# Kernel optimization log

Measured on AMD Instinct MI355X. Metric: run time of the kernel, lower is better.

The kernel has to match this reference:

```python
import jax, jax.numpy as jnp
import numpy as np

B, T = 1, 2048
N_HEAD = 16
N_KV_HEAD = 16
N_EMBD = 1024
HEAD_DIM = N_EMBD // N_HEAD  # 64
HD8 = HEAD_DIM // 8          # 8 octonion blocks per head
EPS_RMS = 1e-6


def qconj(q):
    return q * jnp.array([1.0, -1.0, -1.0, -1.0], dtype=q.dtype)


def qmul(q1, q2):
    # Hamilton product, (...,4) x (...,4) -> (...,4)
    w1, x1, y1, z1 = (q1[..., 0], q1[..., 1], q1[..., 2], q1[..., 3])
    w2, x2, y2, z2 = (q2[..., 0], q2[..., 1], q2[..., 2], q2[..., 3])
    return jnp.stack([
        w1 * w2 - x1 * x2 - y1 * y2 - z1 * z2,
        w1 * x2 + x1 * w2 + y1 * z2 - z1 * y2,
        w1 * y2 - x1 * z2 + y1 * w2 + z1 * x2,
        w1 * z2 + x1 * y2 - y1 * x2 + z1 * w2,
    ], axis=-1)


def omul(o1, o2):
    # Cayley-Dickson octonion product, (...,8)
    a, b = o1[..., :4], o1[..., 4:]
    c, d = o2[..., :4], o2[..., 4:]
    first = qmul(a, c) - qmul(qconj(d), b)
    second = qmul(d, a) + qmul(b, qconj(c))
    return jnp.concatenate([first, second], axis=-1)


def oconj(o):
    return jnp.concatenate([qconj(o[..., :4]), -o[..., 4:]], axis=-1)


# Octonion multiplication structure constants: omul(x, y)[k] = x[a] y[p] C[a,p,k]
_EYE8 = jnp.eye(8, dtype=jnp.float32)
C_OCT = jax.vmap(lambda ei: jax.vmap(lambda ej: omul(ei, ej))(_EYE8))(_EYE8)  # (8,8,8)
# Trilinear tensor for omul(omul(q, kc), v):  T3[a,p,q,k] = sum_e C[a,p,e] C[e,q,k]
T3 = jnp.einsum('ape,eqk->apqk', C_OCT, C_OCT)  # (8,8,8,8)


def apply_rotary_emb(x, cos, sin):
    # x: (B, T, H, hd); cos/sin: (1, T, 1, hd//2)
    d = x.shape[-1] // 2
    x1, x2 = x[..., :d], x[..., d:]
    y1 = x1 * cos + x2 * sin
    y2 = x2 * cos - x1 * sin
    return jnp.concatenate([y1, y2], axis=-1)


def rms_norm(x):
    return x * jax.lax.rsqrt(jnp.mean(x * x, axis=-1, keepdims=True) + EPS_RMS)


def setup_inputs() -> dict:
    key = jax.random.key(0)
    ks = jax.random.split(key, 7)
    x = jax.random.normal(ks[0], (B, T, N_EMBD), dtype=jnp.float32)
    cos = jax.random.uniform(ks[1], (1, T, 1, HEAD_DIM // 2), dtype=jnp.float32)
    sin = jax.random.uniform(ks[2], (1, T, 1, HEAD_DIM // 2), dtype=jnp.float32)
    s = 0.02
    Wq = jax.random.normal(ks[3], (N_HEAD * HEAD_DIM, N_EMBD), dtype=jnp.float32) * s
    Wk = jax.random.normal(ks[4], (N_KV_HEAD * HEAD_DIM, N_EMBD), dtype=jnp.float32) * s
    Wv = jax.random.normal(ks[5], (N_KV_HEAD * HEAD_DIM, N_EMBD), dtype=jnp.float32) * s
    Wo = jax.random.normal(ks[6], (N_EMBD, N_EMBD), dtype=jnp.float32) * s
    return {"x": x, "cos": cos, "sin": sin, "Wq": Wq, "Wk": Wk, "Wv": Wv, "Wo": Wo}


def reference(x, cos, sin, Wq, Wk, Wv, Wo):
    Bx, Tx, Cx = x.shape
    q = (x @ Wq.T).reshape(Bx, Tx, N_HEAD, HEAD_DIM)
    k = (x @ Wk.T).reshape(Bx, Tx, N_KV_HEAD, HEAD_DIM)
    v = (x @ Wv.T).reshape(Bx, Tx, N_KV_HEAD, HEAD_DIM)
    q = rms_norm(apply_rotary_emb(q, cos, sin))
    k = rms_norm(apply_rotary_emb(k, cos, sin))
    q = q.transpose(0, 2, 1, 3)  # (B,H,T,hd)
    k = k.transpose(0, 2, 1, 3)
    v = v.transpose(0, 2, 1, 3)

    q_o = q.reshape(Bx, N_HEAD, Tx, HD8, 8)
    k_o = k.reshape(Bx, N_KV_HEAD, Tx, HD8, 8)
    v_o = v.reshape(Bx, N_KV_HEAD, Tx, HD8, 8)
    # F.normalize(p=2, dim=-1): divide by max(||.||, 1e-12)
    k_o = k_o / jnp.maximum(jnp.linalg.norm(k_o, axis=-1, keepdims=True), 1e-12)

    # Scores use the (pre-octonion-normalized) rotary+rms k
    scores = jnp.einsum('bhid,bhjd->bhij', q, k) * (HEAD_DIM ** -0.5)
    mask = jnp.tril(jnp.ones((Tx, Tx), dtype=bool))
    scores = jnp.where(mask, scores, -jnp.inf)
    probs = jax.nn.softmax(scores, axis=-1)  # (B,H,Tq,Tk)

    # y_i = sum_j p_ij * omul(omul(q_i, oconj(k_j)), v_j)
    # omul is bilinear, so pull the j-sum inside:
    # y_i[k] = q_i[a] * T3[a,p,c,k] * (sum_j p_ij kc_j[p] v_j[c])
    kc = oconj(k_o)                                              # (B,H,Tk,M,8)
    KV = jnp.einsum('bhjmp,bhjmq->bhjmpq', kc, v_o)              # (B,H,Tk,M,8,8)
    Z = jnp.einsum('bhij,bhjmpq->bhimpq', probs, KV)             # (B,H,Tq,M,8,8)
    y_o = jnp.einsum('bhima,apqk,bhimpq->bhimk', q_o, T3, Z)     # (B,H,Tq,M,8)

    y = y_o.reshape(Bx, N_HEAD, Tx, HEAD_DIM).transpose(0, 2, 1, 3).reshape(Bx, Tx, Cx)
    return y @ Wo.T
```

## Files before the change

kernel.cpp:

```cpp
#include <hip/hip_runtime.h>

typedef unsigned short u16;
typedef unsigned int u32;

#define T_SEQ 2048
#define NHEAD 16
#define HDIM 64
#define CDIM 1024
#define W_HSTR (512*2048)
#define Z_HSTR (2048*512)

#define SGBITS 0xB2D8741EACC66A00ULL

#define EXP2C 0.18033688011112042f

typedef _Float16 f16x8 __attribute__((ext_vector_type(8)));
typedef float f32x4 __attribute__((ext_vector_type(4)));

__device__ __forceinline__ float h2f(u16 u) { _Float16 h; __builtin_memcpy(&h, &u, 2); return (float)h; }
__device__ __forceinline__ u16 f2h(float f) { _Float16 h = (_Float16)f; u16 u; __builtin_memcpy(&u, &h, 2); return u; }
__device__ __forceinline__ u32 pk(float a, float b) { return (u32)f2h(a) | ((u32)f2h(b) << 16); }

__device__ __forceinline__ void gload16(const u16* g, u16* l) {
    __builtin_amdgcn_global_load_lds((const __attribute__((address_space(1))) u32*)g,
                                     (__attribute__((address_space(3))) u32*)l, 16, 0, 0);
}

template<bool F16OUT>
__device__ __forceinline__ void hgemm_tile(const u16* __restrict__ At, int lda,
                                           const u16* __restrict__ Bt, int ldb, int K,
                                           float* __restrict__ Cf, u16* __restrict__ Ch,
                                           int ldc, float scale, u16* As, u16* Bs) {
    int t = threadIdx.x;
    int wave = t >> 6, l = t & 63;
    int wm = wave & 1, wn = wave >> 1;
    int quad = l >> 4, lr = l & 15;
    f32x4 acc[4][4];
#pragma unroll
    for (int i = 0; i < 4; ++i)
#pragma unroll
        for (int j = 0; j < 4; ++j) acc[i][j] = (f32x4){0.f, 0.f, 0.f, 0.f};
    int acol = quad * 8;
    for (int k0 = 0; k0 < K; k0 += 64) {
#pragma unroll
        for (int j = 0; j < 4; ++j) {
            int d = wave * 4 + j;
            int kb = d >> 3, seg = d & 7;
            size_t roff = (size_t)(seg * 16 + lr);
            int coff = k0 + kb * 32 + acol;
            gload16(At + roff * lda + coff, As + d * 512);
            gload16(Bt + roff * ldb + coff, Bs + d * 512);
        }
        __syncthreads();
#pragma unroll
        for (int kb = 0; kb < 2; ++kb) {
            f16x8 af[4], bf[4];
#pragma unroll
            for (int mi = 0; mi < 4; ++mi) af[mi] = *(const f16x8*)&As[(kb * 8 + wm * 4 + mi) * 512 + l * 8];
#pragma unroll
            for (int ni = 0; ni < 4; ++ni) bf[ni] = *(const f16x8*)&Bs[(kb * 8 + wn * 4 + ni) * 512 + l * 8];
#pragma unroll
            for (int mi = 0; mi < 4; ++mi)
#pragma unroll
                for (int ni = 0; ni < 4; ++ni)
                    acc[mi][ni] = __builtin_amdgcn_mfma_f32_16x16x32_f16(af[mi], bf[ni], acc[mi][ni], 0, 0, 0);
        }
        __syncthreads();
    }
#pragma unroll
    for (int mi = 0; mi < 4; ++mi)
#pragma unroll
        for (int ni = 0; ni < 4; ++ni)
#pragma unroll
            for (int rr = 0; rr < 4; ++rr) {
                int gr = wm * 64 + mi * 16 + quad * 4 + rr;
                int gc = wn * 64 + ni * 16 + lr;
                float v = acc[mi][ni][rr] * scale;
                if (F16OUT) Ch[(size_t)gr * ldc + gc] = f2h(v);
                else Cf[(size_t)gr * ldc + gc] = v;
            }
}

__global__ __launch_bounds__(256) void hgemm_f32(const u16* __restrict__ A, int lda,
                                                 const u16* __restrict__ B, int ldb,
                                                 float* __restrict__ C, int ldc, int K) {
    __shared__ u16 As[8192], Bs[8192];
    int bm = blockIdx.y * 128, bn = blockIdx.x * 128;
    hgemm_tile<false>(A + (size_t)bm * lda, lda, B + (size_t)bn * ldb, ldb, K,
                      C + (size_t)bm * ldc + bn, nullptr, ldc, 1.f, As, Bs);
}

__global__ __launch_bounds__(256) void hgemm_f16(const u16* __restrict__ A, int lda,
                                                 const u16* __restrict__ B, int ldb,
                                                 u16* __restrict__ C, int ldc, int K) {
    __shared__ u16 As[8192], Bs[8192];
    int bm = blockIdx.y * 128, bn = blockIdx.x * 128;
    hgemm_tile<true>(A + (size_t)bm * lda, lda, B + (size_t)bn * ldb, ldb, K,
                     nullptr, C + (size_t)bm * ldc + bn, ldc, 1.f, As, Bs);
}

__global__ __launch_bounds__(256, 2) void flash_pw(const u16* __restrict__ q16,
                                                   const u16* __restrict__ k16,
                                                   const u16* __restrict__ W,
                                                   u16* __restrict__ Z,
                                                   float* __restrict__ lbuf) {
    __shared__ u16 Pl[2][128 * 136];
    int idx = blockIdx.x;
    int rb = 15 - (idx >> 6);
    int i6 = idx & 63;
    int h = ((i6 & 7) << 1) | ((i6 >> 3) & 1);
    int nq = i6 >> 4;
    int t = threadIdx.x;
    int wave = t >> 6, l = t & 63;
    int wm = wave & 1, wn = wave >> 1;
    int quad = l >> 4, lr = l & 15;

    const u16* qbase = q16 + (size_t)(rb * 128 + wm * 64 + lr) * CDIM + h * HDIM + quad * 8;
    f16x8 qa[4][2];
#pragma unroll
    for (int mi = 0; mi < 4; ++mi)
#pragma unroll
        for (int kb = 0; kb < 2; ++kb)
            qa[mi][kb] = *(const f16x8*)(qbase + (size_t)(mi * 16) * CDIM + kb * 32);

    f32x4 accz[4][4];
    f32x4 accl[4];
#pragma unroll
    for (int mi = 0; mi < 4; ++mi) {
        accl[mi] = (f32x4){0.f, 0.f, 0.f, 0.f};
#pragma unroll
        for (int ni = 0; ni < 4; ++ni) accz[mi][ni] = (f32x4){0.f, 0.f, 0.f, 0.f};
    }
    f16x8 ones;
#pragma unroll
    for (int j = 0; j < 8; ++j) ones[j] = (_Float16)1.0f;

    const u16* kbase = k16 + (size_t)(wn * 64 + lr) * CDIM + h * HDIM + quad * 8;
    const u16* Wbase = W + (size_t)h * W_HSTR + (size_t)(nq * 128 + wn * 64 + lr) * T_SEQ + quad * 8;

    auto qk = [&](int cb, f32x4 (&s)[4][4]) {
        f16x8 kf[4][2];
#pragma unroll
        for (int ni = 0; ni < 4; ++ni)
#pragma unroll
            for (int kb = 0; kb < 2; ++kb)
                kf[ni][kb] = *(const f16x8*)(kbase + (size_t)(cb * 128 + ni * 16) * CDIM + kb * 32);
#pragma unroll
        for (int mi = 0; mi < 4; ++mi)
#pragma unroll
            for (int ni = 0; ni < 4; ++ni) s[mi][ni] = (f32x4){0.f, 0.f, 0.f, 0.f};
#pragma unroll
        for (int kb = 0; kb < 2; ++kb)
#pragma unroll
            for (int mi = 0; mi < 4; ++mi)
#pragma unroll
                for (int ni = 0; ni < 4; ++ni)
                    s[mi][ni] = __builtin_amdgcn_mfma_f32_16x16x32_f16(qa[mi][kb], kf[ni][kb], s[mi][ni], 0, 0, 0);
    };
    auto expst = [&](int cb, f32x4 (&s)[4][4], u16* Pd) {
#pragma unroll
        for (int mi = 0; mi < 4; ++mi) {
            int row = wm * 64 + mi * 16 + quad * 4;
#pragma unroll
            for (int ni = 0; ni < 4; ++ni) {
                int col = wn * 64 + ni * 16 + lr;
#pragma unroll
                for (int rr = 0; rr < 4; ++rr) {
                    bool valid = (cb < rb) | (col <= row + rr);
                    float p = valid ? __builtin_amdgcn_exp2f(s[mi][ni][rr] * EXP2C - 12.f) : 0.f;
                    Pd[(row + rr) * 136 + col] = f2h(p);
                }
            }
        }
    };
    auto pw = [&](int cb, const u16* Ps) {
#pragma unroll
        for (int kb = 0; kb < 4; ++kb) {
            f16x8 pf[4], wf[4];
#pragma unroll
            for (int ni = 0; ni < 4; ++ni)
                wf[ni] = *(const f16x8*)(Wbase + (size_t)(ni * 16) * T_SEQ + cb * 128 + kb * 32);
#pragma unroll
            for (int mi = 0; mi < 4; ++mi)
                pf[mi] = *(const f16x8*)&Ps[(wm * 64 + mi * 16 + lr) * 136 + kb * 32 + quad * 8];
#pragma unroll
            for (int mi = 0; mi < 4; ++mi) {
#pragma unroll
                for (int ni = 0; ni < 4; ++ni)
                    accz[mi][ni] = __builtin_amdgcn_mfma_f32_16x16x32_f16(pf[mi], wf[ni], accz[mi][ni], 0, 0, 0);
                if (nq == 0)
                    accl[mi] = __builtin_amdgcn_mfma_f32_16x16x32_f16(pf[mi], ones, accl[mi], 0, 0, 0);
            }
        }
    };

    {
        f32x4 s[4][4];
        qk(0, s);
        expst(0, s, Pl[0]);
    }
    int cur = 0;
    for (int cb = 1; cb <= rb; ++cb) {
        __syncthreads();
        f32x4 s[4][4];
        qk(cb, s);
        pw(cb - 1, Pl[cur]);
        expst(cb, s, Pl[cur ^ 1]);
        cur ^= 1;
    }
    __syncthreads();
    pw(rb, Pl[cur]);

    u16* Zb = Z + (size_t)h * Z_HSTR;
#pragma unroll
    for (int mi = 0; mi < 4; ++mi)
#pragma unroll
        for (int rr = 0; rr < 4; ++rr) {
            int row = rb * 128 + wm * 64 + mi * 16 + quad * 4 + rr;
#pragma unroll
            for (int ni = 0; ni < 4; ++ni) {
                int col = nq * 128 + wn * 64 + ni * 16 + lr;
                Zb[(size_t)row * 512 + col] = f2h(accz[mi][ni][rr]);
            }
        }
    if (nq == 0 && lr == 0) {
#pragma unroll
        for (int mi = 0; mi < 4; ++mi) {
            int row = rb * 128 + wm * 64 + mi * 16 + quad * 4;
            *(f32x4*)(lbuf + h * T_SEQ + row) = accl[mi];
        }
    }
}

__global__ __launch_bounds__(256) void cvt5(const float* __restrict__ x, const float* __restrict__ wq,
                                            const float* __restrict__ wk, const float* __restrict__ wv,
                                            const float* __restrict__ wo,
                                            u16* __restrict__ x16, u16* __restrict__ w16) {
    int z = blockIdx.y;
    size_t base = ((size_t)blockIdx.x * 256 + threadIdx.x) * 8;
    const float* src;
    u16* dst;
    size_t cnt;
    if (z == 0) { src = x; dst = x16; cnt = 2097152; }
    else if (z == 1) { src = wq; dst = w16; cnt = 1048576; }
    else if (z == 2) { src = wk; dst = w16 + 1048576; cnt = 1048576; }
    else if (z == 3) { src = wv; dst = w16 + 2097152; cnt = 1048576; }
    else { src = wo; dst = w16 + 3145728; cnt = 1048576; }
    if (base >= cnt) return;
    float4 f0 = *(const float4*)(src + base);
    float4 f1 = *(const float4*)(src + base + 4);
    uint4 o;
    o.x = pk(f0.x, f0.y); o.y = pk(f0.z, f0.w); o.z = pk(f1.x, f1.y); o.w = pk(f1.z, f1.w);
    *(uint4*)(dst + base) = o;
}

__global__ __launch_bounds__(256) void prep_rope(const u16* __restrict__ qkv,
                                                 u16* __restrict__ q16, u16* __restrict__ k16,
                                                 float* __restrict__ kc,
                                                 const float* __restrict__ cosb, const float* __restrict__ sinb) {
    int wave = threadIdx.x >> 6, lane = threadIdx.x & 63;
    int idx = blockIdx.x * 4 + wave;
    int t = idx >> 4, h = idx & 15;
    int d = lane & 31;
    float cs = cosb[t * 32 + d];
    float sn = sinb[t * 32 + d];
    size_t b3 = (size_t)t * 3072 + h * HDIM;
    size_t b1 = (size_t)t * CDIM + h * HDIM;

    float xq = h2f(qkv[b3 + lane]);
    float oq = __shfl(xq, lane ^ 32);
    float rq = (lane < 32) ? fmaf(xq, cs, oq * sn) : fmaf(xq, cs, -oq * sn);
    float ssq = rq * rq;
#pragma unroll
    for (int m = 1; m < 64; m <<= 1) ssq += __shfl_xor(ssq, m);
    rq *= rsqrtf(ssq * (1.f / 64.f) + 1e-6f);
    q16[b1 + lane] = f2h(rq);

    float xk = h2f(qkv[b3 + 1024 + lane]);
    float ok = __shfl(xk, lane ^ 32);
    float rk = (lane < 32) ? fmaf(xk, cs, ok * sn) : fmaf(xk, cs, -ok * sn);
    float ssk = rk * rk;
#pragma unroll
    for (int m = 1; m < 64; m <<= 1) ssk += __shfl_xor(ssk, m);
    rk *= rsqrtf(ssk * (1.f / 64.f) + 1e-6f);
    k16[b1 + lane] = f2h(rk);

    float s8 = rk * rk;
    s8 += __shfl_xor(s8, 1); s8 += __shfl_xor(s8, 2); s8 += __shfl_xor(s8, 4);
    float sc2 = 1.f / fmaxf(sqrtf(s8), 1e-12f);
    float kcv = rk * sc2;
    if (lane & 7) kcv = -kcv;
    kc[b1 + lane] = kcv;
}

__global__ __launch_bounds__(256) void w_pre(const float* __restrict__ kc, const u16* __restrict__ qkv,
                                             u16* __restrict__ W) {
    __shared__ float kcs[64][65];
    __shared__ float vs[64][65];
    int h = blockIdx.y;
    int j0 = blockIdx.x * 64;
    int t = threadIdx.x;
    int r = t >> 2, cq = (t & 3) * 16;
    const float* kp = kc + (size_t)(j0 + r) * CDIM + h * HDIM + cq;
    const u16* vp = qkv + (size_t)(j0 + r) * 3072 + 2048 + h * HDIM + cq;
#pragma unroll
    for (int u4 = 0; u4 < 4; ++u4) {
        float4 a = *(const float4*)(kp + u4 * 4);
        ushort4 b = *(const ushort4*)(vp + u4 * 4);
        kcs[r][cq + u4 * 4 + 0] = a.x; kcs[r][cq + u4 * 4 + 1] = a.y;
        kcs[r][cq + u4 * 4 + 2] = a.z; kcs[r][cq + u4 * 4 + 3] = a.w;
        vs[r][cq + u4 * 4 + 0] = h2f(b.x); vs[r][cq + u4 * 4 + 1] = h2f(b.y);
        vs[r][cq + u4 * 4 + 2] = h2f(b.z); vs[r][cq + u4 * 4 + 3] = h2f(b.w);
    }
    __syncthreads();
    int j = t & 63, g = t >> 6;
    u16* Wp = W + (size_t)h * W_HSTR + j0 + j;
    for (int ae = g * 16; ae < g * 16 + 16; ++ae) {
        int a = ae >> 3, e = ae & 7;
        u32 mask = 0;
#pragma unroll
        for (int qq = 0; qq < 8; ++qq) {
            int p = a ^ e ^ qq;
            u32 bit = (u32)(((SGBITS >> (a * 8 + p)) ^ (SGBITS >> ((e ^ qq) * 8 + qq))) & 1ULL);
            mask |= bit << qq;
        }
#pragma unroll
        for (int m = 0; m < 8; ++m) {
            float w = 0.f;
#pragma unroll
            for (int qq = 0; qq < 8; ++qq) {
                float t1 = kcs[j][m * 8 + (a ^ e ^ qq)] * vs[j][m * 8 + qq];
                w = ((mask >> qq) & 1) ? (w - t1) : (w + t1);
            }
            Wp[(size_t)(m * 64 + ae) * T_SEQ] = f2h(w);
        }
    }
}

__global__ __launch_bounds__(256) void contract_y(const u16* __restrict__ q16, const u16* __restrict__ Z,
                                                  const float* __restrict__ lbuf, u16* __restrict__ y16) {
    __shared__ u16 zb[4][512];
    int wave = threadIdx.x >> 6, lane = threadIdx.x & 63;
    int idx = blockIdx.x * 4 + wave;
    int i = idx >> 4, h = idx & 15;
    uint4 zv = *(const uint4*)(Z + (size_t)h * Z_HSTR + (size_t)i * 512 + lane * 8);
    *(uint4*)&zb[wave][lane * 8] = zv;
    int m = lane >> 3, e = lane & 7;
    const u16* qp = q16 + (size_t)i * CDIM + h * HDIM + m * 8;
    uint4 qb = *(const uint4*)qp;
    float qv[8];
    qv[0] = h2f(qb.x & 0xffff); qv[1] = h2f(qb.x >> 16);
    qv[2] = h2f(qb.y & 0xffff); qv[3] = h2f(qb.y >> 16);
    qv[4] = h2f(qb.z & 0xffff); qv[5] = h2f(qb.z >> 16);
    qv[6] = h2f(qb.w & 0xffff); qv[7] = h2f(qb.w >> 16);
    float linv = 1.f / lbuf[h * T_SEQ + i];
    __syncthreads();
    float acc = 0.f;
#pragma unroll
    for (int a = 0; a < 8; ++a) acc = fmaf(qv[a], h2f(zb[wave][m * 64 + a * 8 + e]), acc);
    y16[(size_t)i * CDIM + h * HDIM + lane] = f2h(acc * linv);
}

extern "C" void kernel_launch(void* const* d_in, const int* in_sizes, int n_in,
                              void* d_out, int out_size, void* d_ws, size_t ws_size,
                              hipStream_t stream) {
    const float* x = (const float*)d_in[0];
    const float* cosb = (const float*)d_in[1];
    const float* sinb = (const float*)d_in[2];
    const float* Wq = (const float*)d_in[3];
    const float* Wk = (const float*)d_in[4];
    const float* Wv = (const float*)d_in[5];
    const float* Wo = (const float*)d_in[6];
    float* out = (float*)d_out;
    char* base = (char*)d_ws;
    u16* qkv16 = (u16*)base;
    float* kc = (float*)(base + 12582912);
    u16* x16 = (u16*)(base + 20971520);
    u16* w16 = (u16*)(base + 25165824);
    u16* q16 = (u16*)(base + 33554432);
    u16* k16 = (u16*)(base + 37748736);
    u16* y16 = (u16*)(base + 41943040);
    u16* W = (u16*)(base + 46137344);
    u16* Z = (u16*)(base + 79691776);
    float* lbuf = (float*)(base + 113246208);

    cvt5<<<dim3(1024, 5), 256, 0, stream>>>(x, Wq, Wk, Wv, Wo, x16, w16);
    hgemm_f16<<<dim3(24, 16), 256, 0, stream>>>(x16, CDIM, w16, CDIM, qkv16, 3072, CDIM);
    prep_rope<<<T_SEQ * NHEAD / 4, 256, 0, stream>>>(qkv16, q16, k16, kc, cosb, sinb);
    w_pre<<<dim3(32, 16), 256, 0, stream>>>(kc, qkv16, W);
    flash_pw<<<1024, 256, 0, stream>>>(q16, k16, W, Z, lbuf);
    contract_y<<<NHEAD * T_SEQ / 4, 256, 0, stream>>>(q16, Z, lbuf, y16);
    hgemm_f32<<<dim3(8, 16), 256, 0, stream>>>(y16, CDIM, w16 + 3145728, CDIM, out, CDIM, CDIM);
}
```

Baseline: 305.9 us.

## Share QK/softmax tile across 256 Z columns with 512-thread flash_pw blocks

New measurement: 329.8 us. 1.08x slower.

```diff
diff --git a/kernel.cpp b/kernel.cpp
--- a/kernel.cpp
+++ b/kernel.cpp
@@ -99,17 +99,19 @@
                      nullptr, C + (size_t)bm * ldc + bn, ldc, 1.f, As, Bs);
 }
 
-__global__ __launch_bounds__(256, 2) void flash_pw(const u16* __restrict__ q16,
+__global__ __launch_bounds__(512, 4) void flash_pw(const u16* __restrict__ q16,
                                                    const u16* __restrict__ k16,
                                                    const u16* __restrict__ W,
                                                    u16* __restrict__ Z,
                                                    float* __restrict__ lbuf) {
     __shared__ u16 Pl[2][128 * 136];
     int idx = blockIdx.x;
-    int rb = 15 - (idx >> 6);
-    int i6 = idx & 63;
-    int h = ((i6 & 7) << 1) | ((i6 >> 3) & 1);
-    int nq = i6 >> 4;
+    int pair = idx & 255, half = idx >> 8;
+    int g = pair & 31;
+    int rbh = pair >> 5;
+    int rb = half ? rbh : 15 - rbh;
+    int h = ((g & 7) << 1) | ((g >> 3) & 1);
+    int nq2 = g >> 4;
     int t = threadIdx.x;
     int wave = t >> 6, l = t & 63;
     int wm = wave & 1, wn = wave >> 1;
@@ -135,39 +137,29 @@
 #pragma unroll
     for (int j = 0; j < 8; ++j) ones[j] = (_Float16)1.0f;
 
-    const u16* kbase = k16 + (size_t)(wn * 64 + lr) * CDIM + h * HDIM + quad * 8;
-    const u16* Wbase = W + (size_t)h * W_HSTR + (size_t)(nq * 128 + wn * 64 + lr) * T_SEQ + quad * 8;
-
-    auto qk = [&](int cb, f32x4 (&s)[4][4]) {
-        f16x8 kf[4][2];
-#pragma unroll
-        for (int ni = 0; ni < 4; ++ni)
+    const u16* kbase = k16 + (size_t)(wn * 32 + lr) * CDIM + h * HDIM + quad * 8;
+    const u16* Wbase = W + (size_t)h * W_HSTR + (size_t)(nq2 * 256 + wn * 64 + lr) * T_SEQ + quad * 8;
+
+    auto qk_expst = [&](int cb, u16* Pd) {
+        f16x8 kf[2][2];
+#pragma unroll
+        for (int ni = 0; ni < 2; ++ni)
 #pragma unroll
             for (int kb = 0; kb < 2; ++kb)
                 kf[ni][kb] = *(const f16x8*)(kbase + (size_t)(cb * 128 + ni * 16) * CDIM + kb * 32);
 #pragma unroll
-        for (int mi = 0; mi < 4; ++mi)
-#pragma unroll
-            for (int ni = 0; ni < 4; ++ni) s[mi][ni] = (f32x4){0.f, 0.f, 0.f, 0.f};
-#pragma unroll
-        for (int kb = 0; kb < 2; ++kb)
-#pragma unroll
-            for (int mi = 0; mi < 4; ++mi)
-#pragma unroll
-                for (int ni = 0; ni < 4; ++ni)
-                    s[mi][ni] = __builtin_amdgcn_mfma_f32_16x16x32_f16(qa[mi][kb], kf[ni][kb], s[mi][ni], 0, 0, 0);
-    };
-    auto expst = [&](int cb, f32x4 (&s)[4][4], u16* Pd) {
-#pragma unroll
         for (int mi = 0; mi < 4; ++mi) {
             int row = wm * 64 + mi * 16 + quad * 4;
 #pragma unroll
-            for (int ni = 0; ni < 4; ++ni) {
-                int col = wn * 64 + ni * 16 + lr;
+            for (int ni = 0; ni < 2; ++ni) {
+                f32x4 s = (f32x4){0.f, 0.f, 0.f, 0.f};
+                s = __builtin_amdgcn_mfma_f32_16x16x32_f16(qa[mi][0], kf[ni][0], s, 0, 0, 0);
+                s = __builtin_amdgcn_mfma_f32_16x16x32_f16(qa[mi][1], kf[ni][1], s, 0, 0, 0);
+                int col = wn * 32 + ni * 16 + lr;
 #pragma unroll
                 for (int rr = 0; rr < 4; ++rr) {
                     bool valid = (cb < rb) | (col <= row + rr);
-                    float p = valid ? __builtin_amdgcn_exp2f(s[mi][ni][rr] * EXP2C - 12.f) : 0.f;
+                    float p = valid ? __builtin_amdgcn_exp2f(s[rr] * EXP2C - 12.f) : 0.f;
                     Pd[(row + rr) * 136 + col] = f2h(p);
                 }
             }
@@ -184,28 +176,23 @@
             for (int mi = 0; mi < 4; ++mi)
                 pf[mi] = *(const f16x8*)&Ps[(wm * 64 + mi * 16 + lr) * 136 + kb * 32 + quad * 8];
 #pragma unroll
-            for (int mi = 0; mi < 4; ++mi) {
+            for (int mi = 0; mi < 4; ++mi)
 #pragma unroll
                 for (int ni = 0; ni < 4; ++ni)
                     accz[mi][ni] = __builtin_amdgcn_mfma_f32_16x16x32_f16(pf[mi], wf[ni], accz[mi][ni], 0, 0, 0);
-                if (nq == 0)
+            if (nq2 == 0 && wn == 0)
+#pragma unroll
+                for (int mi = 0; mi < 4; ++mi)
                     accl[mi] = __builtin_amdgcn_mfma_f32_16x16x32_f16(pf[mi], ones, accl[mi], 0, 0, 0);
-            }
         }
     };
 
-    {
-        f32x4 s[4][4];
-        qk(0, s);
-        expst(0, s, Pl[0]);
-    }
+    qk_expst(0, Pl[0]);
     int cur = 0;
     for (int cb = 1; cb <= rb; ++cb) {
         __syncthreads();
-        f32x4 s[4][4];
-        qk(cb, s);
+        qk_expst(cb, Pl[cur ^ 1]);
         pw(cb - 1, Pl[cur]);
-        expst(cb, s, Pl[cur ^ 1]);
         cur ^= 1;
     }
     __syncthreads();
@@ -219,11 +206,11 @@
             int row = rb * 128 + wm * 64 + mi * 16 + quad * 4 + rr;
 #pragma unroll
             for (int ni = 0; ni < 4; ++ni) {
-                int col = nq * 128 + wn * 64 + ni * 16 + lr;
+                int col = nq2 * 256 + wn * 64 + ni * 16 + lr;
                 Zb[(size_t)row * 512 + col] = f2h(accz[mi][ni][rr]);
             }
         }
-    if (nq == 0 && lr == 0) {
+    if (nq2 == 0 && wn == 0 && lr == 0) {
 #pragma unroll
         for (int mi = 0; mi < 4; ++mi) {
             int row = rb * 128 + wm * 64 + mi * 16 + quad * 4;
@@ -388,7 +375,7 @@
     hgemm_f16<<<dim3(24, 16), 256, 0, stream>>>(x16, CDIM, w16, CDIM, qkv16, 3072, CDIM);
     prep_rope<<<T_SEQ * NHEAD / 4, 256, 0, stream>>>(qkv16, q16, k16, kc, cosb, sinb);
     w_pre<<<dim3(32, 16), 256, 0, stream>>>(kc, qkv16, W);
-    flash_pw<<<1024, 256, 0, stream>>>(q16, k16, W, Z, lbuf);
+    flash_pw<<<512, 512, 0, stream>>>(q16, k16, W, Z, lbuf);
     contract_y<<<NHEAD * T_SEQ / 4, 256, 0, stream>>>(q16, Z, lbuf, y16);
     hgemm_f32<<<dim3(8, 16), 256, 0, stream>>>(y16, CDIM, w16 + 3145728, CDIM, out, CDIM, CDIM);
 }
```

## Split fused flash kernel into materialized P tiles and a separate P·W GEMM

Applied to the files above, without the earlier changes.

Result: faster. 283.4 us (-7.3%).

```diff
diff --git a/kernel.cpp b/kernel.cpp
--- a/kernel.cpp
+++ b/kernel.cpp
@@ -9,6 +9,8 @@
 #define CDIM 1024
 #define W_HSTR (512*2048)
 #define Z_HSTR (2048*512)
+#define P_HSTR 2228224
+#define P_TILE 16384
 
 #define SGBITS 0xB2D8741EACC66A00ULL
 
@@ -99,117 +101,134 @@
                      nullptr, C + (size_t)bm * ldc + bn, ldc, 1.f, As, Bs);
 }
 
-__global__ __launch_bounds__(256, 2) void flash_pw(const u16* __restrict__ q16,
-                                                   const u16* __restrict__ k16,
-                                                   const u16* __restrict__ W,
-                                                   u16* __restrict__ Z,
-                                                   float* __restrict__ lbuf) {
-    __shared__ u16 Pl[2][128 * 136];
+__global__ __launch_bounds__(256) void qk_exp_p(const u16* __restrict__ q16,
+                                                const u16* __restrict__ k16,
+                                                u16* __restrict__ P) {
+    __shared__ u16 Pt[128 * 144];
+    int idx = blockIdx.x;
+    int h = idx & 15;
+    int tt = idx >> 4;
+    int rb = 0;
+    while ((rb + 1) * (rb + 2) / 2 <= tt) rb++;
+    int cb = tt - rb * (rb + 1) / 2;
+    int t = threadIdx.x;
+    int wave = t >> 6, l = t & 63;
+    int wm = wave & 1, wn = wave >> 1;
+    int quad = l >> 4, lr = l & 15;
+
+    const u16* qbase = q16 + (size_t)(rb * 128 + wm * 64 + lr) * CDIM + h * HDIM + quad * 8;
+    const u16* kbase = k16 + (size_t)(cb * 128 + wn * 64 + lr) * CDIM + h * HDIM + quad * 8;
+    f16x8 qa[4][2], kf[4][2];
+#pragma unroll
+    for (int mi = 0; mi < 4; ++mi)
+#pragma unroll
+        for (int kb = 0; kb < 2; ++kb)
+            qa[mi][kb] = *(const f16x8*)(qbase + (size_t)(mi * 16) * CDIM + kb * 32);
+#pragma unroll
+    for (int ni = 0; ni < 4; ++ni)
+#pragma unroll
+        for (int kb = 0; kb < 2; ++kb)
+            kf[ni][kb] = *(const f16x8*)(kbase + (size_t)(ni * 16) * CDIM + kb * 32);
+
+    f32x4 s[4][4];
+#pragma unroll
+    for (int mi = 0; mi < 4; ++mi)
+#pragma unroll
+        for (int ni = 0; ni < 4; ++ni) s[mi][ni] = (f32x4){0.f, 0.f, 0.f, 0.f};
+#pragma unroll
+    for (int kb = 0; kb < 2; ++kb)
+#pragma unroll
+        for (int mi = 0; mi < 4; ++mi)
+#pragma unroll
+            for (int ni = 0; ni < 4; ++ni)
+                s[mi][ni] = __builtin_amdgcn_mfma_f32_16x16x32_f16(qa[mi][kb], kf[ni][kb], s[mi][ni], 0, 0, 0);
+
+#pragma unroll
+    for (int mi = 0; mi < 4; ++mi) {
+        int row = wm * 64 + mi * 16 + quad * 4;
+#pragma unroll
+        for (int ni = 0; ni < 4; ++ni) {
+            int col = wn * 64 + ni * 16 + lr;
+#pragma unroll
+            for (int rr = 0; rr < 4; ++rr) {
+                bool valid = (cb < rb) | (col <= row + rr);
+                float p = valid ? __builtin_amdgcn_exp2f(s[mi][ni][rr] * EXP2C - 12.f) : 0.f;
+                Pt[(row + rr) * 144 + col] = f2h(p);
+            }
+        }
+    }
+    __syncthreads();
+    u16* Pg = P + (size_t)h * P_HSTR + (size_t)tt * P_TILE;
+#pragma unroll
+    for (int i = 0; i < 8; ++i) {
+        int c = i * 256 + t;
+        int row = c >> 4, cw = c & 15;
+        uint4 v = *(const uint4*)&Pt[row * 144 + cw * 8];
+        *(uint4*)(Pg + row * 128 + cw * 8) = v;
+    }
+}
+
+__global__ __launch_bounds__(256) void pw_gemm(const u16* __restrict__ P,
+                                               const u16* __restrict__ W,
+                                               u16* __restrict__ Z,
+                                               float* __restrict__ lbuf) {
+    __shared__ u16 As[8192], Bs[8192];
     int idx = blockIdx.x;
     int rb = 15 - (idx >> 6);
     int i6 = idx & 63;
     int h = ((i6 & 7) << 1) | ((i6 >> 3) & 1);
     int nq = i6 >> 4;
+    int K = (rb + 1) * 128;
+    const u16* Ph = P + (size_t)h * P_HSTR + (size_t)(rb * (rb + 1) / 2) * P_TILE;
+    const u16* Bt = W + (size_t)h * W_HSTR + (size_t)(nq * 128) * T_SEQ;
     int t = threadIdx.x;
     int wave = t >> 6, l = t & 63;
     int wm = wave & 1, wn = wave >> 1;
     int quad = l >> 4, lr = l & 15;
-
-    const u16* qbase = q16 + (size_t)(rb * 128 + wm * 64 + lr) * CDIM + h * HDIM + quad * 8;
-    f16x8 qa[4][2];
-#pragma unroll
-    for (int mi = 0; mi < 4; ++mi)
-#pragma unroll
-        for (int kb = 0; kb < 2; ++kb)
-            qa[mi][kb] = *(const f16x8*)(qbase + (size_t)(mi * 16) * CDIM + kb * 32);
-
-    f32x4 accz[4][4];
+    int acol = quad * 8;
+
+    f32x4 acc[4][4];
     f32x4 accl[4];
 #pragma unroll
     for (int mi = 0; mi < 4; ++mi) {
         accl[mi] = (f32x4){0.f, 0.f, 0.f, 0.f};
 #pragma unroll
-        for (int ni = 0; ni < 4; ++ni) accz[mi][ni] = (f32x4){0.f, 0.f, 0.f, 0.f};
+        for (int ni = 0; ni < 4; ++ni) acc[mi][ni] = (f32x4){0.f, 0.f, 0.f, 0.f};
     }
     f16x8 ones;
 #pragma unroll
     for (int j = 0; j < 8; ++j) ones[j] = (_Float16)1.0f;
 
-    const u16* kbase = k16 + (size_t)(wn * 64 + lr) * CDIM + h * HDIM + quad * 8;
-    const u16* Wbase = W + (size_t)h * W_HSTR + (size_t)(nq * 128 + wn * 64 + lr) * T_SEQ + quad * 8;
-
-    auto qk = [&](int cb, f32x4 (&s)[4][4]) {
-        f16x8 kf[4][2];
-#pragma unroll
-        for (int ni = 0; ni < 4; ++ni)
-#pragma unroll
-            for (int kb = 0; kb < 2; ++kb)
-                kf[ni][kb] = *(const f16x8*)(kbase + (size_t)(cb * 128 + ni * 16) * CDIM + kb * 32);
-#pragma unroll
-        for (int mi = 0; mi < 4; ++mi)
-#pragma unroll
-            for (int ni = 0; ni < 4; ++ni) s[mi][ni] = (f32x4){0.f, 0.f, 0.f, 0.f};
-#pragma unroll
-        for (int kb = 0; kb < 2; ++kb)
+    for (int k0 = 0; k0 < K; k0 += 64) {
+        const u16* At = Ph + (size_t)(k0 >> 7) * P_TILE + (k0 & 64);
+#pragma unroll
+        for (int j = 0; j < 4; ++j) {
+            int d = wave * 4 + j;
+            int kb = d >> 3, seg = d & 7;
+            size_t roff = (size_t)(seg * 16 + lr);
+            gload16(At + roff * 128 + kb * 32 + acol, As + d * 512);
+            gload16(Bt + roff * T_SEQ + k0 + kb * 32 + acol, Bs + d * 512);
+        }
+        __syncthreads();
+#pragma unroll
+        for (int kb = 0; kb < 2; ++kb) {
+            f16x8 af[4], bf[4];
+#pragma unroll
+            for (int mi = 0; mi < 4; ++mi) af[mi] = *(const f16x8*)&As[(kb * 8 + wm * 4 + mi) * 512 + l * 8];
+#pragma unroll
+            for (int ni = 0; ni < 4; ++ni) bf[ni] = *(const f16x8*)&Bs[(kb * 8 + wn * 4 + ni) * 512 + l * 8];
 #pragma unroll
             for (int mi = 0; mi < 4; ++mi)
 #pragma unroll
                 for (int ni = 0; ni < 4; ++ni)
-                    s[mi][ni] = __builtin_amdgcn_mfma_f32_16x16x32_f16(qa[mi][kb], kf[ni][kb], s[mi][ni], 0, 0, 0);
-    };
-    auto expst = [&](int cb, f32x4 (&s)[4][4], u16* Pd) {
-#pragma unroll
-        for (int mi = 0; mi < 4; ++mi) {
-            int row = wm * 64 + mi * 16 + quad * 4;
-#pragma unroll
-            for (int ni = 0; ni < 4; ++ni) {
-                int col = wn * 64 + ni * 16 + lr;
-#pragma unroll
-                for (int rr = 0; rr < 4; ++rr) {
-                    bool valid = (cb < rb) | (col <= row + rr);
-                    float p = valid ? __builtin_amdgcn_exp2f(s[mi][ni][rr] * EXP2C - 12.f) : 0.f;
-                    Pd[(row + rr) * 136 + col] = f2h(p);
-                }
-            }
-        }
-    };
-    auto pw = [&](int cb, const u16* Ps) {
-#pragma unroll
-        for (int kb = 0; kb < 4; ++kb) {
-            f16x8 pf[4], wf[4];
-#pragma unroll
-            for (int ni = 0; ni < 4; ++ni)
-                wf[ni] = *(const f16x8*)(Wbase + (size_t)(ni * 16) * T_SEQ + cb * 128 + kb * 32);
-#pragma unroll
-            for (int mi = 0; mi < 4; ++mi)
-                pf[mi] = *(const f16x8*)&Ps[(wm * 64 + mi * 16 + lr) * 136 + kb * 32 + quad * 8];
-#pragma unroll
-            for (int mi = 0; mi < 4; ++mi) {
-#pragma unroll
-                for (int ni = 0; ni < 4; ++ni)
-                    accz[mi][ni] = __builtin_amdgcn_mfma_f32_16x16x32_f16(pf[mi], wf[ni], accz[mi][ni], 0, 0, 0);
-                if (nq == 0)
-                    accl[mi] = __builtin_amdgcn_mfma_f32_16x16x32_f16(pf[mi], ones, accl[mi], 0, 0, 0);
-            }
-        }
-    };
-
-    {
-        f32x4 s[4][4];
-        qk(0, s);
-        expst(0, s, Pl[0]);
-    }
-    int cur = 0;
-    for (int cb = 1; cb <= rb; ++cb) {
+                    acc[mi][ni] = __builtin_amdgcn_mfma_f32_16x16x32_f16(af[mi], bf[ni], acc[mi][ni], 0, 0, 0);
+            if (nq == 0)
+#pragma unroll
+                for (int mi = 0; mi < 4; ++mi)
+                    accl[mi] = __builtin_amdgcn_mfma_f32_16x16x32_f16(af[mi], ones, accl[mi], 0, 0, 0);
+        }
         __syncthreads();
-        f32x4 s[4][4];
-        qk(cb, s);
-        pw(cb - 1, Pl[cur]);
-        expst(cb, s, Pl[cur ^ 1]);
-        cur ^= 1;
-    }
-    __syncthreads();
-    pw(rb, Pl[cur]);
+    }
 
     u16* Zb = Z + (size_t)h * Z_HSTR;
 #pragma unroll
@@ -220,10 +239,10 @@
 #pragma unroll
             for (int ni = 0; ni < 4; ++ni) {
                 int col = nq * 128 + wn * 64 + ni * 16 + lr;
-                Zb[(size_t)row * 512 + col] = f2h(accz[mi][ni][rr]);
+                Zb[(size_t)row * 512 + col] = f2h(acc[mi][ni][rr]);
             }
         }
-    if (nq == 0 && lr == 0) {
+    if (nq == 0 && wn == 0 && lr == 0) {
 #pragma unroll
         for (int mi = 0; mi < 4; ++mi) {
             int row = rb * 128 + wm * 64 + mi * 16 + quad * 4;
@@ -383,12 +402,14 @@
     u16* W = (u16*)(base + 46137344);
     u16* Z = (u16*)(base + 79691776);
     float* lbuf = (float*)(base + 113246208);
+    u16* Pbuf = (u16*)(base + 113377280);
 
     cvt5<<<dim3(1024, 5), 256, 0, stream>>>(x, Wq, Wk, Wv, Wo, x16, w16);
     hgemm_f16<<<dim3(24, 16), 256, 0, stream>>>(x16, CDIM, w16, CDIM, qkv16, 3072, CDIM);
     prep_rope<<<T_SEQ * NHEAD / 4, 256, 0, stream>>>(qkv16, q16, k16, kc, cosb, sinb);
+    qk_exp_p<<<16 * 136, 256, 0, stream>>>(q16, k16, Pbuf);
     w_pre<<<dim3(32, 16), 256, 0, stream>>>(kc, qkv16, W);
-    flash_pw<<<1024, 256, 0, stream>>>(q16, k16, W, Z, lbuf);
+    pw_gemm<<<1024, 256, 0, stream>>>(Pbuf, W, Z, lbuf);
     contract_y<<<NHEAD * T_SEQ / 4, 256, 0, stream>>>(q16, Z, lbuf, y16);
     hgemm_f32<<<dim3(8, 16), 256, 0, stream>>>(y16, CDIM, w16 + 3145728, CDIM, out, CDIM, CDIM);
 }
```
